# Optimization experiments

Hardware: AMD Instinct MI355X
Metric: run time of the kernel (lower is better)

The kernel has to match this reference:

```python
import jax, jax.numpy as jnp
import numpy as np

MODEL_DIM = 256
NUM_HEAD = 8
HEAD_DIM = MODEL_DIM // NUM_HEAD  # 32
ROT_DIM_AXIS = int(0.5 * HEAD_DIM)  # 16 per axis, 32 total rotated channels
LN_EPS = 1e-5
MASK_BIAS = -1e9  # fp32 precision
SCALE = HEAD_DIM ** -0.5
INIT_RANGE = 0.02
N_LAYERS = 6


def _rotate_half(x):
    # interleaved pairs: (d r) with r=2 -> (-x2, x1) re-interleaved
    x = x.reshape(*x.shape[:-1], -1, 2)
    x1, x2 = x[..., 0], x[..., 1]
    return jnp.stack([-x2, x1], axis=-1).reshape(*x.shape[:-2], -1)


def _axial_freqs(seqlen):
    # RotaryEmbedding('lang' freqs) over t = linspace(-1, 1, seqlen)
    inv_freq = 1.0 / (10000.0 ** (jnp.arange(0, ROT_DIM_AXIS, 2, dtype=jnp.float32) / ROT_DIM_AXIS))
    t = jnp.linspace(-1.0, 1.0, seqlen, dtype=jnp.float32)
    f = jnp.repeat(t[:, None] * inv_freq[None, :], 2, axis=-1)  # (s, ROT_DIM_AXIS)
    fh = jnp.broadcast_to(f[:, None, :], (seqlen, seqlen, ROT_DIM_AXIS))
    fw = jnp.broadcast_to(f[None, :, :], (seqlen, seqlen, ROT_DIM_AXIS))
    return jnp.concatenate([fh, fw], axis=-1)  # (s, s, 2*ROT_DIM_AXIS)


def _apply_rotary(freqs, t):
    rot_dim = freqs.shape[-1]
    t_rot, t_pass = t[..., :rot_dim], t[..., rot_dim:]
    t_rot = t_rot * jnp.cos(freqs) + _rotate_half(t_rot) * jnp.sin(freqs)
    return jnp.concatenate([t_rot, t_pass], axis=-1)


def setup_inputs() -> dict:
    key = jax.random.key(0)
    k1, k2, k3, k4 = jax.random.split(key, 4)
    b, s = 2, 128
    pair_act = jax.random.normal(k1, (b, s, s, MODEL_DIM), dtype=jnp.float32)
    pair_mask = jax.random.randint(k2, (b, s, s), 0, 2).astype(bool)  # True = masked
    Wqkv = jax.random.normal(k3, (3 * MODEL_DIM, MODEL_DIM), dtype=jnp.float32) * INIT_RANGE
    Wout = jax.random.normal(k4, (MODEL_DIM, MODEL_DIM), dtype=jnp.float32) * (INIT_RANGE / np.sqrt(2 * N_LAYERS))
    ln_gamma = jnp.ones((MODEL_DIM,), dtype=jnp.float32)
    ln_beta = jnp.zeros((MODEL_DIM,), dtype=jnp.float32)
    return {"pair_act": pair_act, "pair_mask": pair_mask, "ln_gamma": ln_gamma,
            "ln_beta": ln_beta, "Wqkv": Wqkv, "Wout": Wout}


def reference(pair_act, pair_mask, ln_gamma, ln_beta, Wqkv, Wout):
    # orientation == 'per_row': no axis swap
    b, s = pair_act.shape[0], pair_act.shape[1]
    # LayerNorm over model_dim
    mu = jnp.mean(pair_act, axis=-1, keepdims=True)
    var = jnp.var(pair_act, axis=-1, keepdims=True)
    x = (pair_act - mu) * jax.lax.rsqrt(var + LN_EPS) * ln_gamma + ln_beta
    # QKV projection (no bias)
    qkv = jnp.einsum('bxyd,ed->bxye', x, Wqkv)  # (b, s, s, 3*MODEL_DIM)
    q, k, v = jnp.split(qkv, 3, axis=-1)
    # 2D axial rotary on first 2*ROT_DIM_AXIS channels of the feature dim
    freqs = _axial_freqs(s)  # (s, s, 32)
    q = _apply_rotary(freqs, q)
    k = _apply_rotary(freqs, k)
    # multihead attention per row (axis s1 independent)
    q = q.reshape(b, s, s, NUM_HEAD, HEAD_DIM)
    k = k.reshape(b, s, s, NUM_HEAD, HEAD_DIM)
    v = v.reshape(b, s, s, NUM_HEAD, HEAD_DIM)
    scores = jnp.einsum('bxqhd,bxkhd->bxhqk', q, k) * SCALE  # (b, s1, h, s2, s2)
    mask = pair_mask[:, :, None, None, :]  # (b, s1, 1, 1, s2)
    scores = jnp.where(mask, MASK_BIAS, scores)
    attn = jax.nn.softmax(scores, axis=-1)
    out = jnp.einsum('bxhqk,bxkhd->bxqhd', attn, v).reshape(b, s, s, MODEL_DIM)
    return jnp.einsum('bxyd,ed->bxye', out, Wout)
```

## Files before the change

### kernel.cpp

```cpp
#include <hip/hip_runtime.h>
#include <math.h>
#include <stdint.h>

typedef __attribute__((ext_vector_type(8))) short short8;
typedef __attribute__((ext_vector_type(4))) float floatx4;

#define LN_EPS 1e-5f
#define ATT_SCALE 0.17677669529663687f

__device__ __constant__ float INVF[8] = {
    1.0f, 0.31622776601683794f, 0.1f, 0.031622776601683794f,
    0.01f, 0.0031622776601683794f, 0.001f, 0.00031622776601683794f};

__device__ inline unsigned short f2bf(float f) {
    unsigned u = __float_as_uint(f);
    u += 0x7fffu + ((u >> 16) & 1u);
    return (unsigned short)(u >> 16);
}

__device__ inline void gl_lds16(const unsigned short* g, unsigned short* l) {
    __builtin_amdgcn_global_load_lds(
        (const __attribute__((address_space(1))) void*)(uintptr_t)g,
        (__attribute__((address_space(3))) void*)(uintptr_t)l, 16, 0, 0);
}

__global__ __launch_bounds__(256)
void prep_w(const float* __restrict__ wq, const float* __restrict__ wo,
            unsigned short* __restrict__ bq, unsigned short* __restrict__ bo) {
    int g = blockIdx.x * 256 + threadIdx.x;
    const float* src;
    unsigned short* dst;
    if (g < 49152) { src = wq + (size_t)g * 4; dst = bq + (size_t)g * 4; }
    else { int h = g - 49152; src = wo + (size_t)h * 4; dst = bo + (size_t)h * 4; }
    float4 v = *(const float4*)src;
    uint2 o;
    o.x = (unsigned)f2bf(v.x) | ((unsigned)f2bf(v.y) << 16);
    o.y = (unsigned)f2bf(v.z) | ((unsigned)f2bf(v.w) << 16);
    *(uint2*)dst = o;
}

__global__ __launch_bounds__(512, 2)
void fused_kernel(const float* __restrict__ pair_act, const int* __restrict__ mask,
                  const float* __restrict__ gamma, const float* __restrict__ beta,
                  const unsigned short* __restrict__ Wqkv,
                  const unsigned short* __restrict__ Wout,
                  float* __restrict__ out) {
    __shared__ __align__(16) unsigned char smem[61952];
    unsigned short* S16 = (unsigned short*)smem;
    unsigned short* Ks = (unsigned short*)(smem + 32768);
    unsigned short* Vt = (unsigned short*)(smem + 43008);

    int bx = blockIdx.x;
    int tid = threadIdx.x;
    int w = tid >> 6, lane = tid & 63, qd = lane >> 4, lo = lane & 15;
    unsigned short* Qscr = (unsigned short*)(smem + 51712) + w * 640;

    float tX = -1.0f + (2.0f / 127.0f) * (float)(bx & 127);

    short8 a_frag[8];
    #pragma unroll
    for (int p = 0; p < 2; ++p) {
        if (tid < 256) {
            int rl = tid >> 2, q0 = tid & 3;
            const float* src = pair_act + ((size_t)(bx * 128 + p * 64 + rl)) * 256;
            float4 v[16];
            float s = 0.f;
            #pragma unroll
            for (int u = 0; u < 16; ++u) {
                v[u] = *(const float4*)(src + q0 * 4 + u * 16);
                s += v[u].x + v[u].y + v[u].z + v[u].w;
            }
            s += __shfl_xor(s, 1);
            s += __shfl_xor(s, 2);
            float mean = s * (1.0f / 256.0f);
            float sq = 0.f;
            #pragma unroll
            for (int u = 0; u < 16; ++u) {
                float d0 = v[u].x - mean, d1 = v[u].y - mean;
                float d2 = v[u].z - mean, d3 = v[u].w - mean;
                sq += d0 * d0 + d1 * d1 + d2 * d2 + d3 * d3;
            }
            sq += __shfl_xor(sq, 1);
            sq += __shfl_xor(sq, 2);
            float rs = rsqrtf(sq * (1.0f / 256.0f) + LN_EPS);
            #pragma unroll
            for (int u = 0; u < 16; ++u) {
                float4 g4 = *(const float4*)(gamma + q0 * 4 + u * 16);
                float4 b4 = *(const float4*)(beta + q0 * 4 + u * 16);
                unsigned e0 = f2bf((v[u].x - mean) * rs * g4.x + b4.x);
                unsigned e1 = f2bf((v[u].y - mean) * rs * g4.y + b4.y);
                unsigned e2 = f2bf((v[u].z - mean) * rs * g4.z + b4.z);
                unsigned e3 = f2bf((v[u].w - mean) * rs * g4.w + b4.w);
                int c = 2 * u + (q0 >> 1);
                int half = q0 & 1;
                int ss = (c & ~7) | ((c & 7) ^ (rl & 7));
                uint2 pk = {e0 | (e1 << 16), e2 | (e3 << 16)};
                *(uint2*)&S16[rl * 256 + ss * 8 + half * 4] = pk;
            }
        }
        __syncthreads();
        if ((w >> 2) == p) {
            int rl = (w & 3) * 16 + lo;
            #pragma unroll
            for (int c = 0; c < 8; ++c) {
                int ci = 4 * c + qd;
                int ss = (ci & ~7) | ((ci & 7) ^ (rl & 7));
                a_frag[c] = *(const short8*)&S16[rl * 256 + ss * 8];
            }
        }
        __syncthreads();
    }

    unsigned q_pk[4][4][2], k_pk[4][4][2], v_pk[4][4][2];
    #pragma unroll
    for (int nc = 0; nc < 12; ++nc) {
        #pragma unroll
        for (int i = 0; i < 4; ++i) {
            int rbase = i * 16 + w * 2;
            int row = rbase + (lane >> 5);
            int sl = lane & 31;
            int c = (sl & ~7) | ((sl & 7) ^ (row & 7));
            gl_lds16(Wqkv + (size_t)(nc * 64 + row) * 256 + c * 8, S16 + rbase * 256);
        }
        __syncthreads();
        floatx4 acc[4];
        #pragma unroll
        for (int t = 0; t < 4; ++t) acc[t] = (floatx4){0.f, 0.f, 0.f, 0.f};
        #pragma unroll
        for (int c = 0; c < 8; ++c) {
            #pragma unroll
            for (int t = 0; t < 4; ++t) {
                int rw = t * 16 + lo;
                int ci = 4 * c + qd;
                int ss = (ci & ~7) | ((ci & 7) ^ (rw & 7));
                short8 bf = *(const short8*)&S16[rw * 256 + ss * 8];
                acc[t] = __builtin_amdgcn_mfma_f32_16x16x32_bf16(a_frag[c], bf,
                                                                 acc[t], 0, 0, 0);
            }
        }
        __syncthreads();
        if (nc == 0 || nc == 4) {
            #pragma unroll
            for (int t = 0; t < 2; ++t) {
                int pi = (t * 16 + lo) >> 1;
                float invf = INVF[pi & 7];
                float sgn = (lo & 1) ? 1.0f : -1.0f;
                #pragma unroll
                for (int r = 0; r < 4; ++r) {
                    int y = 16 * w + qd * 4 + r;
                    float tp = (pi < 8) ? tX : (-1.0f + (2.0f / 127.0f) * (float)y);
                    float sn, cs;
                    __sincosf(tp * invf, &sn, &cs);
                    float vv = acc[t][r];
                    float pv = __shfl_xor(vv, 1);
                    acc[t][r] = vv * cs + sgn * pv * sn;
                }
            }
        }
        #pragma unroll
        for (int t = 0; t < 4; ++t) {
            unsigned p0 = (unsigned)f2bf(acc[t][0]) | ((unsigned)f2bf(acc[t][1]) << 16);
            unsigned p1 = (unsigned)f2bf(acc[t][2]) | ((unsigned)f2bf(acc[t][3]) << 16);
            if (nc < 4) { q_pk[nc][t][0] = p0; q_pk[nc][t][1] = p1; }
            else if (nc < 8) { k_pk[nc - 4][t][0] = p0; k_pk[nc - 4][t][1] = p1; }
            else { v_pk[nc - 8][t][0] = p0; v_pk[nc - 8][t][1] = p1; }
        }
    }

    float msel[8];
    #pragma unroll
    for (int nt = 0; nt < 8; ++nt)
        msel[nt] = mask[bx * 128 + nt * 16 + lo] ? 0.0f : 1.0f;

    unsigned o_pk[8][2][2];
    #pragma unroll
    for (int h = 0; h < 8; ++h) {
        int hc = h >> 1, tt0 = (h & 1) * 2;
        #pragma unroll
        for (int tt = 0; tt < 2; ++tt) {
            int t = tt0 + tt;
            #pragma unroll
            for (int r = 0; r < 4; ++r) {
                unsigned kv = (k_pk[hc][t][r >> 1] >> ((r & 1) * 16)) & 0xffffu;
                unsigned vv = (v_pk[hc][t][r >> 1] >> ((r & 1) * 16)) & 0xffffu;
                int key = 16 * w + qd * 4 + r;
                int d = tt * 16 + lo;
                Ks[key * 40 + d] = (unsigned short)kv;
                Vt[d * 136 + key] = (unsigned short)vv;
            }
        }
        __syncthreads();
        #pragma unroll
        for (int tt = 0; tt < 2; ++tt) {
            int t = tt0 + tt;
            #pragma unroll
            for (int r = 0; r < 4; ++r) {
                unsigned qv = (q_pk[hc][t][r >> 1] >> ((r & 1) * 16)) & 0xffffu;
                Qscr[(qd * 4 + r) * 40 + tt * 16 + lo] = (unsigned short)qv;
            }
        }
        short8 aq = *(const short8*)&Qscr[lo * 40 + qd * 8];
        float ef[8][4];
        float sums[4] = {0.f, 0.f, 0.f, 0.f};
        #pragma unroll
        for (int nt = 0; nt < 8; ++nt) {
            short8 bk = *(const short8*)&Ks[(nt * 16 + lo) * 40 + qd * 8];
            floatx4 c = (floatx4){0.f, 0.f, 0.f, 0.f};
            c = __builtin_amdgcn_mfma_f32_16x16x32_bf16(aq, bk, c, 0, 0, 0);
            #pragma unroll
            for (int r = 0; r < 4; ++r) {
                float e = __expf(c[r] * ATT_SCALE) * msel[nt];
                ef[nt][r] = e;
                sums[r] += e;
            }
        }
        float inv[4];
        #pragma unroll
        for (int r = 0; r < 4; ++r) {
            float v = sums[r];
            v += __shfl_xor(v, 1);
            v += __shfl_xor(v, 2);
            v += __shfl_xor(v, 4);
            v += __shfl_xor(v, 8);
            inv[r] = 1.0f / v;
        }
        floatx4 o[2];
        o[0] = (floatx4){0.f, 0.f, 0.f, 0.f};
        o[1] = (floatx4){0.f, 0.f, 0.f, 0.f};
        #pragma unroll
        for (int c2 = 0; c2 < 4; ++c2) {
            #pragma unroll
            for (int half = 0; half < 2; ++half) {
                int nt = c2 * 2 + half;
                #pragma unroll
                for (int r = 0; r < 4; ++r)
                    Qscr[(qd * 4 + r) * 40 + half * 16 + lo] = f2bf(ef[nt][r]);
            }
            short8 pa = *(const short8*)&Qscr[lo * 40 + qd * 8];
            #pragma unroll
            for (int n = 0; n < 2; ++n) {
                short8 vb = *(const short8*)&Vt[(n * 16 + lo) * 136 + c2 * 32 + qd * 8];
                o[n] = __builtin_amdgcn_mfma_f32_16x16x32_bf16(pa, vb, o[n], 0, 0, 0);
            }
        }
        #pragma unroll
        for (int n = 0; n < 2; ++n) {
            o_pk[h][n][0] = (unsigned)f2bf(o[n][0] * inv[0]) |
                            ((unsigned)f2bf(o[n][1] * inv[1]) << 16);
            o_pk[h][n][1] = (unsigned)f2bf(o[n][2] * inv[2]) |
                            ((unsigned)f2bf(o[n][3] * inv[3]) << 16);
        }
        __syncthreads();
    }

    short8 of[8];
    #pragma unroll
    for (int h = 0; h < 8; ++h) {
        #pragma unroll
        for (int tt = 0; tt < 2; ++tt)
            #pragma unroll
            for (int r = 0; r < 4; ++r) {
                unsigned ov = (o_pk[h][tt][r >> 1] >> ((r & 1) * 16)) & 0xffffu;
                Qscr[(qd * 4 + r) * 40 + tt * 16 + lo] = (unsigned short)ov;
            }
        of[h] = *(const short8*)&Qscr[lo * 40 + qd * 8];
    }
    #pragma unroll
    for (int nc = 0; nc < 4; ++nc) {
        #pragma unroll
        for (int i = 0; i < 4; ++i) {
            int rbase = i * 16 + w * 2;
            int row = rbase + (lane >> 5);
            int sl = lane & 31;
            int c = (sl & ~7) | ((sl & 7) ^ (row & 7));
            gl_lds16(Wout + (size_t)(nc * 64 + row) * 256 + c * 8, S16 + rbase * 256);
        }
        __syncthreads();
        floatx4 acc[4];
        #pragma unroll
        for (int t = 0; t < 4; ++t) acc[t] = (floatx4){0.f, 0.f, 0.f, 0.f};
        #pragma unroll
        for (int c = 0; c < 8; ++c) {
            #pragma unroll
            for (int t = 0; t < 4; ++t) {
                int rw = t * 16 + lo;
                int ci = 4 * c + qd;
                int ss = (ci & ~7) | ((ci & 7) ^ (rw & 7));
                short8 bf = *(const short8*)&S16[rw * 256 + ss * 8];
                acc[t] = __builtin_amdgcn_mfma_f32_16x16x32_bf16(of[c], bf,
                                                                 acc[t], 0, 0, 0);
            }
        }
        #pragma unroll
        for (int t = 0; t < 4; ++t)
            #pragma unroll
            for (int r = 0; r < 4; ++r)
                out[(size_t)(bx * 128 + 16 * w + qd * 4 + r) * 256 + nc * 64 +
                    t * 16 + lo] = acc[t][r];
        __syncthreads();
    }
}

extern "C" void kernel_launch(void* const* d_in, const int* in_sizes, int n_in,
                              void* d_out, int out_size, void* d_ws, size_t ws_size,
                              hipStream_t stream) {
    const float* pair_act = (const float*)d_in[0];
    const int* pair_mask = (const int*)d_in[1];
    const float* ln_gamma = (const float*)d_in[2];
    const float* ln_beta = (const float*)d_in[3];
    const float* Wqkv = (const float*)d_in[4];
    const float* Wout = (const float*)d_in[5];
    float* out = (float*)d_out;

    char* ws = (char*)d_ws;
    unsigned short* wqkv_bf = (unsigned short*)ws;
    unsigned short* wout_bf = (unsigned short*)(ws + 393216);

    prep_w<<<256, 256, 0, stream>>>(Wqkv, Wout, wqkv_bf, wout_bf);
    fused_kernel<<<256, 512, 0, stream>>>(pair_act, pair_mask, ln_gamma, ln_beta,
                                          wqkv_bf, wout_bf, out);
}
```

Before: 156.9 us.

## Interleave QKV projection with per-head attention to cut register pressure

Restructures the fused kernel so each pair of heads computes its Q, K and V projection chunk right before its attention, instead of holding all Q/K/V for every head in registers. The layernorm now uses all 512 threads in one pass, writing the normalized row in two halves, and the mask load is hoisted to the start. Attention output fragments go straight into the A-operand registers for the output projection, which removes the packed o_pk array. The aim is lower VGPR pressure and fewer spills at 2 blocks per CU, at the cost of reordering barriers and some added synchronisation.

```diff
diff --git a/kernel.cpp b/kernel.cpp
--- a/kernel.cpp
+++ b/kernel.cpp
@@ -45,249 +45,249 @@
                   const unsigned short* __restrict__ Wqkv,
                   const unsigned short* __restrict__ Wout,
                   float* __restrict__ out) {
-    __shared__ __align__(16) unsigned char smem[61952];
-    unsigned short* S16 = (unsigned short*)smem;
-    unsigned short* Ks = (unsigned short*)(smem + 32768);
-    unsigned short* Vt = (unsigned short*)(smem + 43008);
+    __shared__ __align__(16) unsigned short S16[16384];
+    __shared__ __align__(16) unsigned short Ks[128 * 40];
+    __shared__ __align__(16) unsigned short Vt[32 * 136];
+    __shared__ __align__(16) unsigned short Qall[8 * 640];
 
     int bx = blockIdx.x;
     int tid = threadIdx.x;
     int w = tid >> 6, lane = tid & 63, qd = lane >> 4, lo = lane & 15;
-    unsigned short* Qscr = (unsigned short*)(smem + 51712) + w * 640;
+    unsigned short* Qscr = Qall + w * 640;
 
     float tX = -1.0f + (2.0f / 127.0f) * (float)(bx & 127);
 
+    float msel[8];
+    #pragma unroll
+    for (int nt = 0; nt < 8; ++nt)
+        msel[nt] = mask[bx * 128 + nt * 16 + lo] ? 0.0f : 1.0f;
+
     short8 a_frag[8];
-    #pragma unroll
-    for (int p = 0; p < 2; ++p) {
-        if (tid < 256) {
-            int rl = tid >> 2, q0 = tid & 3;
-            const float* src = pair_act + ((size_t)(bx * 128 + p * 64 + rl)) * 256;
-            float4 v[16];
-            float s = 0.f;
-            #pragma unroll
-            for (int u = 0; u < 16; ++u) {
-                v[u] = *(const float4*)(src + q0 * 4 + u * 16);
-                s += v[u].x + v[u].y + v[u].z + v[u].w;
-            }
-            s += __shfl_xor(s, 1);
-            s += __shfl_xor(s, 2);
-            float mean = s * (1.0f / 256.0f);
-            float sq = 0.f;
-            #pragma unroll
-            for (int u = 0; u < 16; ++u) {
-                float d0 = v[u].x - mean, d1 = v[u].y - mean;
-                float d2 = v[u].z - mean, d3 = v[u].w - mean;
-                sq += d0 * d0 + d1 * d1 + d2 * d2 + d3 * d3;
-            }
-            sq += __shfl_xor(sq, 1);
-            sq += __shfl_xor(sq, 2);
-            float rs = rsqrtf(sq * (1.0f / 256.0f) + LN_EPS);
-            #pragma unroll
-            for (int u = 0; u < 16; ++u) {
+    {
+        int rl = tid >> 2, q0 = tid & 3;
+        const float* src = pair_act + ((size_t)(bx * 128 + rl)) * 256 + q0 * 4;
+        float4 v[16];
+        float s = 0.f;
+        #pragma unroll
+        for (int u = 0; u < 16; ++u) {
+            v[u] = *(const float4*)(src + u * 16);
+            s += v[u].x + v[u].y + v[u].z + v[u].w;
+        }
+        s += __shfl_xor(s, 1);
+        s += __shfl_xor(s, 2);
+        float mean = s * (1.0f / 256.0f);
+        float sq = 0.f;
+        #pragma unroll
+        for (int u = 0; u < 16; ++u) {
+            float d0 = v[u].x - mean, d1 = v[u].y - mean;
+            float d2 = v[u].z - mean, d3 = v[u].w - mean;
+            sq += d0 * d0 + d1 * d1 + d2 * d2 + d3 * d3;
+        }
+        sq += __shfl_xor(sq, 1);
+        sq += __shfl_xor(sq, 2);
+        float rs = rsqrtf(sq * (1.0f / 256.0f) + LN_EPS);
+
+        int rw = 16 * w + lo;
+        #pragma unroll
+        for (int p = 0; p < 2; ++p) {
+            #pragma unroll
+            for (int ul = 0; ul < 8; ++ul) {
+                int u = p * 8 + ul;
                 float4 g4 = *(const float4*)(gamma + q0 * 4 + u * 16);
                 float4 b4 = *(const float4*)(beta + q0 * 4 + u * 16);
                 unsigned e0 = f2bf((v[u].x - mean) * rs * g4.x + b4.x);
                 unsigned e1 = f2bf((v[u].y - mean) * rs * g4.y + b4.y);
                 unsigned e2 = f2bf((v[u].z - mean) * rs * g4.z + b4.z);
                 unsigned e3 = f2bf((v[u].w - mean) * rs * g4.w + b4.w);
-                int c = 2 * u + (q0 >> 1);
-                int half = q0 & 1;
-                int ss = (c & ~7) | ((c & 7) ^ (rl & 7));
-                uint2 pk = {e0 | (e1 << 16), e2 | (e3 << 16)};
-                *(uint2*)&S16[rl * 256 + ss * 8 + half * 4] = pk;
-            }
-        }
+                int cw = 2 * ul + (q0 >> 1);
+                int ss = (cw & ~7) | ((cw & 7) ^ (rl & 7));
+                uint2 pk;
+                pk.x = e0 | (e1 << 16);
+                pk.y = e2 | (e3 << 16);
+                *(uint2*)&S16[rl * 128 + ss * 8 + (q0 & 1) * 4] = pk;
+            }
+            __syncthreads();
+            #pragma unroll
+            for (int cp = 0; cp < 4; ++cp) {
+                int ci = cp * 4 + qd;
+                int ss = (ci & ~7) | ((ci & 7) ^ (rw & 7));
+                a_frag[p * 4 + cp] = *(const short8*)&S16[rw * 128 + ss * 8];
+            }
+            __syncthreads();
+        }
+    }
+
+    short8 of[8];
+    #pragma unroll
+    for (int hc = 0; hc < 4; ++hc) {
+        unsigned q_pk[4][2], k_pk[4][2], v_pk[4][2];
+        #pragma unroll
+        for (int part = 0; part < 3; ++part) {
+            if (hc != 0 || part != 0) __syncthreads();
+            const unsigned short* Wsrc = Wqkv + (size_t)(part * 256 + hc * 64) * 256;
+            #pragma unroll
+            for (int i = 0; i < 4; ++i) {
+                int rbase = i * 16 + w * 2;
+                int row = rbase + (lane >> 5);
+                int sl = lane & 31;
+                int c = (sl & ~7) | ((sl & 7) ^ (row & 7));
+                gl_lds16(Wsrc + (size_t)row * 256 + c * 8, S16 + rbase * 256);
+            }
+            __syncthreads();
+            floatx4 acc[4];
+            #pragma unroll
+            for (int t = 0; t < 4; ++t) acc[t] = (floatx4){0.f, 0.f, 0.f, 0.f};
+            #pragma unroll
+            for (int cc = 0; cc < 8; ++cc) {
+                #pragma unroll
+                for (int t = 0; t < 4; ++t) {
+                    int rw2 = t * 16 + lo;
+                    int ci = cc * 4 + qd;
+                    int ss = (ci & ~7) | ((ci & 7) ^ (rw2 & 7));
+                    short8 bf = *(const short8*)&S16[rw2 * 256 + ss * 8];
+                    acc[t] = __builtin_amdgcn_mfma_f32_16x16x32_bf16(
+                        a_frag[cc], bf, acc[t], 0, 0, 0);
+                }
+            }
+            if (hc == 0 && part < 2) {
+                #pragma unroll
+                for (int t = 0; t < 2; ++t) {
+                    int pi = (t * 16 + lo) >> 1;
+                    float invf = INVF[pi & 7];
+                    float sgn = (lo & 1) ? 1.0f : -1.0f;
+                    #pragma unroll
+                    for (int r = 0; r < 4; ++r) {
+                        int y = 16 * w + qd * 4 + r;
+                        float tp = (pi < 8) ? tX
+                                            : (-1.0f + (2.0f / 127.0f) * (float)y);
+                        float sn, cs;
+                        __sincosf(tp * invf, &sn, &cs);
+                        float vv = acc[t][r];
+                        float pv = __shfl_xor(vv, 1);
+                        acc[t][r] = vv * cs + sgn * pv * sn;
+                    }
+                }
+            }
+            #pragma unroll
+            for (int t = 0; t < 4; ++t) {
+                unsigned p0 = (unsigned)f2bf(acc[t][0]) |
+                              ((unsigned)f2bf(acc[t][1]) << 16);
+                unsigned p1 = (unsigned)f2bf(acc[t][2]) |
+                              ((unsigned)f2bf(acc[t][3]) << 16);
+                if (part == 0) { q_pk[t][0] = p0; q_pk[t][1] = p1; }
+                else if (part == 1) { k_pk[t][0] = p0; k_pk[t][1] = p1; }
+                else { v_pk[t][0] = p0; v_pk[t][1] = p1; }
+            }
+        }
+
+        #pragma unroll
+        for (int sub = 0; sub < 2; ++sub) {
+            int h = hc * 2 + sub, tt0 = sub * 2;
+            __syncthreads();
+            #pragma unroll
+            for (int tt = 0; tt < 2; ++tt) {
+                int t = tt0 + tt;
+                int d = tt * 16 + lo;
+                #pragma unroll
+                for (int r = 0; r < 4; ++r) {
+                    unsigned kv = (k_pk[t][r >> 1] >> ((r & 1) * 16)) & 0xffffu;
+                    Ks[(16 * w + qd * 4 + r) * 40 + d] = (unsigned short)kv;
+                }
+                uint2 pv;
+                pv.x = v_pk[t][0];
+                pv.y = v_pk[t][1];
+                *(uint2*)&Vt[d * 136 + 16 * w + qd * 4] = pv;
+            }
+            __syncthreads();
+            #pragma unroll
+            for (int tt = 0; tt < 2; ++tt) {
+                int t = tt0 + tt;
+                #pragma unroll
+                for (int r = 0; r < 4; ++r) {
+                    unsigned qv = (q_pk[t][r >> 1] >> ((r & 1) * 16)) & 0xffffu;
+                    Qscr[(qd * 4 + r) * 40 + tt * 16 + lo] = (unsigned short)qv;
+                }
+            }
+            short8 aq = *(const short8*)&Qscr[lo * 40 + qd * 8];
+            float ef[8][4];
+            float sums[4] = {0.f, 0.f, 0.f, 0.f};
+            #pragma unroll
+            for (int nt = 0; nt < 8; ++nt) {
+                short8 bk = *(const short8*)&Ks[(nt * 16 + lo) * 40 + qd * 8];
+                floatx4 c = (floatx4){0.f, 0.f, 0.f, 0.f};
+                c = __builtin_amdgcn_mfma_f32_16x16x32_bf16(aq, bk, c, 0, 0, 0);
+                #pragma unroll
+                for (int r = 0; r < 4; ++r) {
+                    float e = __expf(c[r] * ATT_SCALE) * msel[nt];
+                    ef[nt][r] = e;
+                    sums[r] += e;
+                }
+            }
+            float inv[4];
+            #pragma unroll
+            for (int r = 0; r < 4; ++r) {
+                float vv = sums[r];
+                vv += __shfl_xor(vv, 1);
+                vv += __shfl_xor(vv, 2);
+                vv += __shfl_xor(vv, 4);
+                vv += __shfl_xor(vv, 8);
+                inv[r] = 1.0f / vv;
+            }
+            floatx4 o[2];
+            o[0] = (floatx4){0.f, 0.f, 0.f, 0.f};
+            o[1] = (floatx4){0.f, 0.f, 0.f, 0.f};
+            #pragma unroll
+            for (int c2 = 0; c2 < 4; ++c2) {
+                #pragma unroll
+                for (int half = 0; half < 2; ++half) {
+                    int nt = c2 * 2 + half;
+                    #pragma unroll
+                    for (int r = 0; r < 4; ++r)
+                        Qscr[(qd * 4 + r) * 40 + half * 16 + lo] = f2bf(ef[nt][r]);
+                }
+                short8 pa = *(const short8*)&Qscr[lo * 40 + qd * 8];
+                #pragma unroll
+                for (int n = 0; n < 2; ++n) {
+                    short8 vb =
+                        *(const short8*)&Vt[(n * 16 + lo) * 136 + c2 * 32 + qd * 8];
+                    o[n] = __builtin_amdgcn_mfma_f32_16x16x32_bf16(pa, vb, o[n],
+                                                                   0, 0, 0);
+                }
+            }
+            #pragma unroll
+            for (int n = 0; n < 2; ++n)
+                #pragma unroll
+                for (int r = 0; r < 4; ++r)
+                    Qscr[(qd * 4 + r) * 40 + n * 16 + lo] = f2bf(o[n][r] * inv[r]);
+            of[h] = *(const short8*)&Qscr[lo * 40 + qd * 8];
+        }
+    }
+
+    #pragma unroll
+    for (int nc = 0; nc < 4; ++nc) {
         __syncthreads();
-        if ((w >> 2) == p) {
-            int rl = (w & 3) * 16 + lo;
-            #pragma unroll
-            for (int c = 0; c < 8; ++c) {
-                int ci = 4 * c + qd;
-                int ss = (ci & ~7) | ((ci & 7) ^ (rl & 7));
-                a_frag[c] = *(const short8*)&S16[rl * 256 + ss * 8];
-            }
-        }
-        __syncthreads();
-    }
-
-    unsigned q_pk[4][4][2], k_pk[4][4][2], v_pk[4][4][2];
-    #pragma unroll
-    for (int nc = 0; nc < 12; ++nc) {
+        const unsigned short* Wsrc = Wout + (size_t)(nc * 64) * 256;
         #pragma unroll
         for (int i = 0; i < 4; ++i) {
             int rbase = i * 16 + w * 2;
             int row = rbase + (lane >> 5);
             int sl = lane & 31;
             int c = (sl & ~7) | ((sl & 7) ^ (row & 7));
-            gl_lds16(Wqkv + (size_t)(nc * 64 + row) * 256 + c * 8, S16 + rbase * 256);
+            gl_lds16(Wsrc + (size_t)row * 256 + c * 8, S16 + rbase * 256);
         }
         __syncthreads();
         floatx4 acc[4];
         #pragma unroll
         for (int t = 0; t < 4; ++t) acc[t] = (floatx4){0.f, 0.f, 0.f, 0.f};
         #pragma unroll
-        for (int c = 0; c < 8; ++c) {
+        for (int cc = 0; cc < 8; ++cc) {
             #pragma unroll
             for (int t = 0; t < 4; ++t) {
-                int rw = t * 16 + lo;
-                int ci = 4 * c + qd;
-                int ss = (ci & ~7) | ((ci & 7) ^ (rw & 7));
-                short8 bf = *(const short8*)&S16[rw * 256 + ss * 8];
-                acc[t] = __builtin_amdgcn_mfma_f32_16x16x32_bf16(a_frag[c], bf,
-                                                                 acc[t], 0, 0, 0);
-            }
-        }
-        __syncthreads();
-        if (nc == 0 || nc == 4) {
-            #pragma unroll
-            for (int t = 0; t < 2; ++t) {
-                int pi = (t * 16 + lo) >> 1;
-                float invf = INVF[pi & 7];
-                float sgn = (lo & 1) ? 1.0f : -1.0f;
-                #pragma unroll
-                for (int r = 0; r < 4; ++r) {
-                    int y = 16 * w + qd * 4 + r;
-                    float tp = (pi < 8) ? tX : (-1.0f + (2.0f / 127.0f) * (float)y);
-                    float sn, cs;
-                    __sincosf(tp * invf, &sn, &cs);
-                    float vv = acc[t][r];
-                    float pv = __shfl_xor(vv, 1);
-                    acc[t][r] = vv * cs + sgn * pv * sn;
-                }
-            }
-        }
-        #pragma unroll
-        for (int t = 0; t < 4; ++t) {
-            unsigned p0 = (unsigned)f2bf(acc[t][0]) | ((unsigned)f2bf(acc[t][1]) << 16);
-            unsigned p1 = (unsigned)f2bf(acc[t][2]) | ((unsigned)f2bf(acc[t][3]) << 16);
-            if (nc < 4) { q_pk[nc][t][0] = p0; q_pk[nc][t][1] = p1; }
-            else if (nc < 8) { k_pk[nc - 4][t][0] = p0; k_pk[nc - 4][t][1] = p1; }
-            else { v_pk[nc - 8][t][0] = p0; v_pk[nc - 8][t][1] = p1; }
-        }
-    }
-
-    float msel[8];
-    #pragma unroll
-    for (int nt = 0; nt < 8; ++nt)
-        msel[nt] = mask[bx * 128 + nt * 16 + lo] ? 0.0f : 1.0f;
-
-    unsigned o_pk[8][2][2];
-    #pragma unroll
-    for (int h = 0; h < 8; ++h) {
-        int hc = h >> 1, tt0 = (h & 1) * 2;
-        #pragma unroll
-        for (int tt = 0; tt < 2; ++tt) {
-            int t = tt0 + tt;
-            #pragma unroll
-            for (int r = 0; r < 4; ++r) {
-                unsigned kv = (k_pk[hc][t][r >> 1] >> ((r & 1) * 16)) & 0xffffu;
-                unsigned vv = (v_pk[hc][t][r >> 1] >> ((r & 1) * 16)) & 0xffffu;
-                int key = 16 * w + qd * 4 + r;
-                int d = tt * 16 + lo;
-                Ks[key * 40 + d] = (unsigned short)kv;
-                Vt[d * 136 + key] = (unsigned short)vv;
-            }
-        }
-        __syncthreads();
-        #pragma unroll
-        for (int tt = 0; tt < 2; ++tt) {
-            int t = tt0 + tt;
-            #pragma unroll
-            for (int r = 0; r < 4; ++r) {
-                unsigned qv = (q_pk[hc][t][r >> 1] >> ((r & 1) * 16)) & 0xffffu;
-                Qscr[(qd * 4 + r) * 40 + tt * 16 + lo] = (unsigned short)qv;
-            }
-        }
-        short8 aq = *(const short8*)&Qscr[lo * 40 + qd * 8];
-        float ef[8][4];
-        float sums[4] = {0.f, 0.f, 0.f, 0.f};
-        #pragma unroll
-        for (int nt = 0; nt < 8; ++nt) {
-            short8 bk = *(const short8*)&Ks[(nt * 16 + lo) * 40 + qd * 8];
-            floatx4 c = (floatx4){0.f, 0.f, 0.f, 0.f};
-            c = __builtin_amdgcn_mfma_f32_16x16x32_bf16(aq, bk, c, 0, 0, 0);
-            #pragma unroll
-            for (int r = 0; r < 4; ++r) {
-                float e = __expf(c[r] * ATT_SCALE) * msel[nt];
-                ef[nt][r] = e;
-                sums[r] += e;
-            }
-        }
-        float inv[4];
-        #pragma unroll
-        for (int r = 0; r < 4; ++r) {
-            float v = sums[r];
-            v += __shfl_xor(v, 1);
-            v += __shfl_xor(v, 2);
-            v += __shfl_xor(v, 4);
-            v += __shfl_xor(v, 8);
-            inv[r] = 1.0f / v;
-        }
-        floatx4 o[2];
-        o[0] = (floatx4){0.f, 0.f, 0.f, 0.f};
-        o[1] = (floatx4){0.f, 0.f, 0.f, 0.f};
-        #pragma unroll
-        for (int c2 = 0; c2 < 4; ++c2) {
-            #pragma unroll
-            for (int half = 0; half < 2; ++half) {
-                int nt = c2 * 2 + half;
-                #pragma unroll
-                for (int r = 0; r < 4; ++r)
-                    Qscr[(qd * 4 + r) * 40 + half * 16 + lo] = f2bf(ef[nt][r]);
-            }
-            short8 pa = *(const short8*)&Qscr[lo * 40 + qd * 8];
-            #pragma unroll
-            for (int n = 0; n < 2; ++n) {
-                short8 vb = *(const short8*)&Vt[(n * 16 + lo) * 136 + c2 * 32 + qd * 8];
-                o[n] = __builtin_amdgcn_mfma_f32_16x16x32_bf16(pa, vb, o[n], 0, 0, 0);
-            }
-        }
-        #pragma unroll
-        for (int n = 0; n < 2; ++n) {
-            o_pk[h][n][0] = (unsigned)f2bf(o[n][0] * inv[0]) |
-                            ((unsigned)f2bf(o[n][1] * inv[1]) << 16);
-            o_pk[h][n][1] = (unsigned)f2bf(o[n][2] * inv[2]) |
-                            ((unsigned)f2bf(o[n][3] * inv[3]) << 16);
-        }
-        __syncthreads();
-    }
-
-    short8 of[8];
-    #pragma unroll
-    for (int h = 0; h < 8; ++h) {
-        #pragma unroll
-        for (int tt = 0; tt < 2; ++tt)
-            #pragma unroll
-            for (int r = 0; r < 4; ++r) {
-                unsigned ov = (o_pk[h][tt][r >> 1] >> ((r & 1) * 16)) & 0xffffu;
-                Qscr[(qd * 4 + r) * 40 + tt * 16 + lo] = (unsigned short)ov;
-            }
-        of[h] = *(const short8*)&Qscr[lo * 40 + qd * 8];
-    }
-    #pragma unroll
-    for (int nc = 0; nc < 4; ++nc) {
-        #pragma unroll
-        for (int i = 0; i < 4; ++i) {
-            int rbase = i * 16 + w * 2;
-            int row = rbase + (lane >> 5);
-            int sl = lane & 31;
-            int c = (sl & ~7) | ((sl & 7) ^ (row & 7));
-            gl_lds16(Wout + (size_t)(nc * 64 + row) * 256 + c * 8, S16 + rbase * 256);
-        }
-        __syncthreads();
-        floatx4 acc[4];
-        #pragma unroll
-        for (int t = 0; t < 4; ++t) acc[t] = (floatx4){0.f, 0.f, 0.f, 0.f};
-        #pragma unroll
-        for (int c = 0; c < 8; ++c) {
-            #pragma unroll
-            for (int t = 0; t < 4; ++t) {
-                int rw = t * 16 + lo;
-                int ci = 4 * c + qd;
-                int ss = (ci & ~7) | ((ci & 7) ^ (rw & 7));
-                short8 bf = *(const short8*)&S16[rw * 256 + ss * 8];
-                acc[t] = __builtin_amdgcn_mfma_f32_16x16x32_bf16(of[c], bf,
+                int rw2 = t * 16 + lo;
+                int ci = cc * 4 + qd;
+                int ss = (ci & ~7) | ((ci & 7) ^ (rw2 & 7));
+                short8 bf = *(const short8*)&S16[rw2 * 256 + ss * 8];
+                acc[t] = __builtin_amdgcn_mfma_f32_16x16x32_bf16(of[cc], bf,
                                                                  acc[t], 0, 0, 0);
             }
         }
@@ -297,7 +297,6 @@
             for (int r = 0; r < 4; ++r)
                 out[(size_t)(bx * 128 + 16 * w + qd * 4 + r) * 256 + nc * 64 +
                     t * 16 + lo] = acc[t][r];
-        __syncthreads();
     }
 }
 
```

After: 138.9 us. 11.4% less time.
